# Optimization experiments

Measured on AMD Instinct MI355X. Metric: run time of the kernel, lower is better.

Reference implementation:

```python
import jax, jax.numpy as jnp
import numpy as np

B, S, D, H = 4, 2048, 1024, 16  # batch, seq, d_hidden, n_heads


def setup_inputs() -> dict:
    key = jax.random.key(0)
    ks = jax.random.split(key, 7)
    scale = 1.0 / np.sqrt(D)
    return {
        "x": jax.random.normal(ks[0], (B, S, D), dtype=jnp.float32),
        "Wq": jax.random.normal(ks[1], (D, D), dtype=jnp.float32) * scale,
        "bq": jax.random.normal(ks[2], (D,), dtype=jnp.float32) * 0.02,
        "Wk": jax.random.normal(ks[3], (D, D), dtype=jnp.float32) * scale,
        "bk": jax.random.normal(ks[4], (D,), dtype=jnp.float32) * 0.02,
        "Wv": jax.random.normal(ks[5], (D, D), dtype=jnp.float32) * scale,
        "bv": jax.random.normal(ks[6], (D,), dtype=jnp.float32) * 0.02,
    }


def reference(x, Wq, bq, Wk, bk, Wv, bv):
    n_heads = H
    head_dim = D // n_heads

    def proj(inp, W, b):
        # torch nn.Linear: y = x @ W^T + b
        y = jnp.einsum("bsd,ed->bse", inp, W) + b
        # split last dim into (H, Wd) then transpose to (B, H, S, Wd)
        return y.reshape(inp.shape[0], inp.shape[1], n_heads, head_dim).transpose(0, 2, 1, 3)

    q = proj(x, Wq, bq)
    k = proj(x, Wk, bk)
    v = proj(x, Wv, bv)

    # scores: (B, H, S, S)
    scores = jnp.einsum("bhqd,bhkd->bhqk", q, k) / jnp.sqrt(jnp.asarray(head_dim, q.dtype))
    attn = jax.nn.softmax(scores, axis=-1)
    h = jnp.einsum("bhqk,bhkd->bhqd", attn, v)  # (B, H, S, Wd)
    h = h.transpose(0, 2, 1, 3).reshape(x.shape[0], x.shape[1], D)  # merge heads
    return h
```

## Files before the change

### kernel.cpp

```cpp
#include <hip/hip_runtime.h>
#include <hip/hip_bf16.h>

#define B_ 4
#define S_ 2048
#define D_ 1024
#define H_ 16
#define HD 64

typedef __bf16 bf16;
typedef __bf16 bf16x4 __attribute__((ext_vector_type(4)));
typedef __bf16 bf16x8 __attribute__((ext_vector_type(8)));
typedef float f32x4 __attribute__((ext_vector_type(4)));
typedef float f32x16 __attribute__((ext_vector_type(16)));

#define LOG2E 1.4426950408889634f

__device__ inline void gload_lds16(const bf16* g, bf16* l) {
    __builtin_amdgcn_global_load_lds(
        (const __attribute__((address_space(1))) void*)g,
        (__attribute__((address_space(3))) void*)l, 16, 0, 0);
}

__device__ inline int swz(int row, int colb) {
    return row * 64 + ((colb ^ ((row & 7) << 4)) >> 1);
}

__device__ inline unsigned cvt_pk_bf16(float lo, float hi) {
    unsigned r;
    asm("v_cvt_pk_bf16_f32 %0, %1, %2" : "=v"(r) : "v"(lo), "v"(hi));
    return r;
}

__global__ void cast_pack_kernel(const float* __restrict__ x,
                                 const float* __restrict__ Wq,
                                 const float* __restrict__ Wk,
                                 const float* __restrict__ Wv,
                                 bf16* __restrict__ Xb, bf16* __restrict__ Wb) {
    const long XN = (long)B_ * S_ * D_;
    const long WN = (long)D_ * D_;
    long i4 = ((long)blockIdx.x * blockDim.x + threadIdx.x) * 4;
    if (i4 < XN) {
        float4 v = *(const float4*)(x + i4);
        bf16* o = Xb + i4;
        o[0] = (bf16)v.x; o[1] = (bf16)v.y; o[2] = (bf16)v.z; o[3] = (bf16)v.w;
    } else {
        long j = i4 - XN;
        if (j < 3 * WN) {
            int which = (int)(j / WN);
            long jj = j - (long)which * WN;
            const float* src = which == 0 ? Wq : which == 1 ? Wk : Wv;
            float4 v = *(const float4*)(src + jj);
            bf16* o = Wb + j;
            o[0] = (bf16)v.x; o[1] = (bf16)v.y; o[2] = (bf16)v.z; o[3] = (bf16)v.w;
        }
    }
}

#define TM 128
#define TN 256
#define TK 64

__global__ __launch_bounds__(512, 2) void gemm_qkv_kernel(
    const bf16* __restrict__ Xb, const bf16* __restrict__ Wb,
    const float* __restrict__ bq, const float* __restrict__ bk,
    const float* __restrict__ bv,
    bf16* __restrict__ Qg, bf16* __restrict__ Kg, bf16* __restrict__ Vt) {
    __shared__ bf16 SMEM[49152];
    bf16* As = SMEM;
    bf16* Bs = SMEM + 16384;
    const int tid = threadIdx.x;
    const int lane = tid & 63;
    const int wid = tid >> 6;
    const int col = lane & 15, grp = lane >> 4;
    const int wr = wid >> 2, wc = wid & 3;

    const int id = blockIdx.x;
    const int id2 = (id & 7) * 96 + (id >> 3);
    const int m0 = (id2 / 12) * TM;
    const int n0 = (id2 % 12) * TN;

    const int r8 = tid >> 3;
    const int cbs = ((tid & 7) * 16) ^ ((r8 & 7) << 4);
    const bf16* asrc = Xb + (size_t)(m0 + r8) * D_ + (cbs >> 1);
    const bf16* bsrc = Wb + (size_t)(n0 + r8) * D_ + (cbs >> 1);

#define STAGE_A(c, kt, j) \
    gload_lds16(asrc + (size_t)(j) * 64 * D_ + (kt) * TK, As + (c) * 8192 + (j) * 4096 + wid * 512)
#define STAGE_B(c, kt, j) \
    gload_lds16(bsrc + (size_t)(j) * 64 * D_ + (kt) * TK, Bs + (c) * 16384 + (j) * 4096 + wid * 512)

    const f32x4 zf = {0.f, 0.f, 0.f, 0.f};
    f32x4 acc[4][4];
#pragma unroll
    for (int m = 0; m < 4; m++)
#pragma unroll
        for (int n = 0; n < 4; n++) acc[m][n] = zf;

    STAGE_A(0, 0, 0); STAGE_A(0, 0, 1);
    STAGE_B(0, 0, 0); STAGE_B(0, 0, 1); STAGE_B(0, 0, 2); STAGE_B(0, 0, 3);
    asm volatile("s_waitcnt vmcnt(0)");
    __builtin_amdgcn_s_barrier();

    int c = 0;
#pragma unroll 1
    for (int kt = 0; kt < D_ / TK; ++kt) {
        const bf16* Ac = As + c * 8192;
        const bf16* Bc = Bs + c * 16384;
        {
            bf16x8 a[4], b[4];
#pragma unroll
            for (int m = 0; m < 4; m++)
                a[m] = *(const bf16x8*)(Ac + swz(wr * 64 + m * 16 + col, grp * 16));
#pragma unroll
            for (int n = 0; n < 4; n++)
                b[n] = *(const bf16x8*)(Bc + swz(wc * 64 + n * 16 + col, grp * 16));
            if (kt < D_ / TK - 1) {
                STAGE_A(c ^ 1, kt + 1, 0); STAGE_A(c ^ 1, kt + 1, 1);
                STAGE_B(c ^ 1, kt + 1, 0);
            }
            __builtin_amdgcn_s_barrier();
            asm volatile("s_waitcnt lgkmcnt(0)");
            __builtin_amdgcn_sched_barrier(0);
            __builtin_amdgcn_s_setprio(1);
#pragma unroll
            for (int m = 0; m < 4; m++)
#pragma unroll
                for (int n = 0; n < 4; n++)
                    acc[m][n] = __builtin_amdgcn_mfma_f32_16x16x32_bf16(a[m], b[n], acc[m][n], 0, 0, 0);
            __builtin_amdgcn_s_setprio(0);
            __builtin_amdgcn_s_barrier();
        }
        {
            bf16x8 a[4], b[4];
#pragma unroll
            for (int m = 0; m < 4; m++)
                a[m] = *(const bf16x8*)(Ac + swz(wr * 64 + m * 16 + col, 64 + grp * 16));
#pragma unroll
            for (int n = 0; n < 4; n++)
                b[n] = *(const bf16x8*)(Bc + swz(wc * 64 + n * 16 + col, 64 + grp * 16));
            if (kt < D_ / TK - 1) {
                STAGE_B(c ^ 1, kt + 1, 1); STAGE_B(c ^ 1, kt + 1, 2); STAGE_B(c ^ 1, kt + 1, 3);
            }
            __builtin_amdgcn_s_barrier();
            asm volatile("s_waitcnt lgkmcnt(0)");
            __builtin_amdgcn_sched_barrier(0);
            __builtin_amdgcn_s_setprio(1);
#pragma unroll
            for (int m = 0; m < 4; m++)
#pragma unroll
                for (int n = 0; n < 4; n++)
                    acc[m][n] = __builtin_amdgcn_mfma_f32_16x16x32_bf16(a[m], b[n], acc[m][n], 0, 0, 0);
            __builtin_amdgcn_s_setprio(0);
            asm volatile("s_waitcnt vmcnt(0)");
            __builtin_amdgcn_s_barrier();
        }
        c ^= 1;
    }
#undef STAGE_A
#undef STAGE_B

    const int which = n0 >> 10;
    if (which == 2) {
        __syncthreads();
        bf16* Vl = SMEM;
#pragma unroll
        for (int n = 0; n < 4; n++) {
            int dl = wc * 64 + n * 16 + col;
            float bias = bv[(n0 - 2048) + dl];
#pragma unroll
            for (int m = 0; m < 4; m++) {
                bf16x4 pv;
#pragma unroll
                for (int i = 0; i < 4; i++) pv[i] = (bf16)(acc[m][n][i] + bias);
                int sl = wr * 64 + m * 16 + grp * 4;
                *(bf16x4*)(&Vl[dl * 128 + (sl ^ ((dl & 7) << 3))]) = pv;
            }
        }
        __syncthreads();
#pragma unroll
        for (int c0 = 0; c0 < 8; c0++) {
            int cc = c0 * 512 + tid;
            int dl = cc >> 4, s8 = (cc & 15) * 8;
            bf16x8 val = *(const bf16x8*)(&Vl[dl * 128 + (s8 ^ ((dl & 7) << 3))]);
            int s = m0 + s8;
            int b = s >> 11, sl = s & 2047;
            int dglob = (n0 - 2048) + dl;
            int h = dglob >> 6, dd = dglob & 63;
            *(bf16x8*)(&Vt[((size_t)(b * H_ + h) * HD + dd) * S_ + sl]) = val;
        }
    } else {
        const float* bp = which == 0 ? bq : bk;
        bf16* dst = which == 0 ? Qg : Kg;
        const float qsc = which == 0 ? (0.125f * LOG2E) : 1.0f;
#pragma unroll
        for (int n = 0; n < 4; n++) {
            int e = n0 + wc * 64 + n * 16 + col;
            int ee = e & 1023;
            float bias = bp[ee];
            int h = ee >> 6, d = ee & 63;
#pragma unroll
            for (int m = 0; m < 4; m++) {
#pragma unroll
                for (int i = 0; i < 4; i++) {
                    int s = m0 + wr * 64 + m * 16 + grp * 4 + i;
                    int b = s >> 11, sl = s & 2047;
                    dst[((size_t)(b * H_ + h) * S_ + sl) * HD + d] =
                        (bf16)((acc[m][n][i] + bias) * qsc);
                }
            }
        }
    }
}

#define KB 64

__global__ __launch_bounds__(256, 4) void attn_kernel(
    const bf16* __restrict__ Qg, const bf16* __restrict__ Kg,
    const bf16* __restrict__ Vt, float* __restrict__ out) {
    __shared__ bf16 Ks[2][64 * 64];
    __shared__ bf16 Vs[2][64 * 64];
    const int tid = threadIdx.x, lane = tid & 63, wid = tid >> 6;
    const int l31 = lane & 31, hi = lane >> 5;

    const int id = blockIdx.x;
    const int swzid = (id & 7) * 128 + (id >> 3);
    const int bh = swzid >> 4;
    const int q0 = (swzid & 15) * 128 + wid * 32;

    const bf16* Kbase = Kg + (size_t)bh * S_ * HD;
    const bf16* Vbase = Vt + (size_t)bh * HD * S_;

    const int r0 = tid >> 3;
    const int cb = ((tid & 7) * 16) ^ ((r0 & 7) << 4);
    const bf16* ksrc = Kbase + (size_t)r0 * HD + (cb >> 1);
    const bf16* vsrc = Vbase + (size_t)r0 * S_ + (cb >> 1);

#define STAGE(bsel, kv0)                                                       \
    do {                                                                       \
        gload_lds16(ksrc + (size_t)(kv0)*HD,        &Ks[bsel][wid * 512]);     \
        gload_lds16(ksrc + (size_t)((kv0) + 32)*HD, &Ks[bsel][2048 + wid * 512]); \
        gload_lds16(vsrc + (kv0),                   &Vs[bsel][wid * 512]);     \
        gload_lds16(vsrc + 32 * S_ + (kv0),         &Vs[bsel][2048 + wid * 512]); \
    } while (0)

    bf16x8 qa[4];
#pragma unroll
    for (int ks = 0; ks < 4; ks++)
        qa[ks] = *(const bf16x8*)(Qg + ((size_t)bh * S_ + q0 + l31) * HD + ks * 16 + hi * 8);

    const f32x16 z16 = {0.f, 0.f, 0.f, 0.f, 0.f, 0.f, 0.f, 0.f,
                        0.f, 0.f, 0.f, 0.f, 0.f, 0.f, 0.f, 0.f};
    f32x16 o[2];
    o[0] = z16; o[1] = z16;
    f32x4 ls = {0.f, 0.f, 0.f, 0.f};

    int cur = 0;
    STAGE(0, 0);
    __syncthreads();

#pragma unroll 1
    for (int t = 0; t < S_ / KB; ++t) {
        if (t < S_ / KB - 1) STAGE(cur ^ 1, (t + 1) * KB);

        f32x16 sc[2];
        __builtin_amdgcn_s_setprio(1);
#pragma unroll
        for (int kvt = 0; kvt < 2; kvt++) {
#pragma unroll
            for (int ks = 0; ks < 4; ks++) {
                bf16x8 kb = *(const bf16x8*)(&Ks[cur][swz(kvt * 32 + l31, ks * 32 + hi * 16)]);
                if (ks == 0)
                    sc[kvt] = __builtin_amdgcn_mfma_f32_32x32x16_bf16(kb, qa[0], z16, 0, 0, 0);
                else
                    sc[kvt] = __builtin_amdgcn_mfma_f32_32x32x16_bf16(kb, qa[ks], sc[kvt], 0, 0, 0);
            }
        }
        __builtin_amdgcn_s_setprio(0);

#pragma unroll
        for (int kvt = 0; kvt < 2; kvt++) {
            float p[16];
#pragma unroll
            for (int r = 0; r < 16; r++) p[r] = __builtin_amdgcn_exp2f(sc[kvt][r]);
            f32x4 s0 = {p[0], p[1], p[2], p[3]};
            f32x4 s1 = {p[4], p[5], p[6], p[7]};
            f32x4 s2 = {p[8], p[9], p[10], p[11]};
            f32x4 s3 = {p[12], p[13], p[14], p[15]};
            ls += (s0 + s1) + (s2 + s3);
            bf16x8 pa[2];
#pragma unroll
            for (int b = 0; b < 2; b++) {
                unsigned A  = cvt_pk_bf16(p[8 * b + 0], p[8 * b + 1]);
                unsigned Bw = cvt_pk_bf16(p[8 * b + 4], p[8 * b + 5]);
                unsigned C  = cvt_pk_bf16(p[8 * b + 2], p[8 * b + 3]);
                unsigned Dw = cvt_pk_bf16(p[8 * b + 6], p[8 * b + 7]);
                asm("v_permlane32_swap_b32 %0, %1" : "+v"(A), "+v"(Bw));
                asm("v_permlane32_swap_b32 %0, %1" : "+v"(C), "+v"(Dw));
                union { unsigned u[4]; bf16x8 v; } pk;
                pk.u[0] = A; pk.u[1] = C; pk.u[2] = Bw; pk.u[3] = Dw;
                pa[b] = pk.v;
            }
            __builtin_amdgcn_s_setprio(1);
#pragma unroll
            for (int b = 0; b < 2; b++) {
                int kk = kvt * 2 + b;
                bf16x8 vb0 = *(const bf16x8*)(&Vs[cur][swz(l31,      kk * 32 + hi * 16)]);
                bf16x8 vb1 = *(const bf16x8*)(&Vs[cur][swz(32 + l31, kk * 32 + hi * 16)]);
                o[0] = __builtin_amdgcn_mfma_f32_32x32x16_bf16(vb0, pa[b], o[0], 0, 0, 0);
                o[1] = __builtin_amdgcn_mfma_f32_32x32x16_bf16(vb1, pa[b], o[1], 0, 0, 0);
            }
            __builtin_amdgcn_s_setprio(0);
        }

        __syncthreads();
        cur ^= 1;
    }

    float denom = ls[0] + ls[1] + ls[2] + ls[3];
    denom += __shfl_xor(denom, 32);
    float inv = 1.f / denom;

    int b = bh >> 4, h = bh & 15;
    int q = q0 + l31;
    float* obase = out + ((size_t)(b * S_ + q)) * D_ + h * HD;
#pragma unroll
    for (int dt = 0; dt < 2; dt++)
#pragma unroll
        for (int g = 0; g < 4; g++) {
            f32x4 r = {o[dt][4 * g + 0] * inv, o[dt][4 * g + 1] * inv,
                       o[dt][4 * g + 2] * inv, o[dt][4 * g + 3] * inv};
            *(f32x4*)(obase + dt * 32 + 8 * g + 4 * hi) = r;
        }
#undef STAGE
}

extern "C" void kernel_launch(void* const* d_in, const int* in_sizes, int n_in,
                              void* d_out, int out_size, void* d_ws, size_t ws_size,
                              hipStream_t stream) {
    const float* x  = (const float*)d_in[0];
    const float* Wq = (const float*)d_in[1];
    const float* bq = (const float*)d_in[2];
    const float* Wk = (const float*)d_in[3];
    const float* bk = (const float*)d_in[4];
    const float* Wv = (const float*)d_in[5];
    const float* bv = (const float*)d_in[6];
    float* out = (float*)d_out;

    bf16* ws = (bf16*)d_ws;
    bf16* Xb = ws;
    bf16* Wb = Xb + (size_t)B_ * S_ * D_;
    bf16* Qg = Wb + (size_t)3 * D_ * D_;
    bf16* Kg = Qg + (size_t)B_ * S_ * D_;
    bf16* Vt = Kg + (size_t)B_ * S_ * D_;

    hipLaunchKernelGGL(cast_pack_kernel,
                       dim3((B_ * S_ * D_ + 3 * D_ * D_) / (4 * 256)), dim3(256), 0, stream,
                       x, Wq, Wk, Wv, Xb, Wb);
    hipLaunchKernelGGL(gemm_qkv_kernel, dim3(64 * 12), dim3(512), 0, stream,
                       Xb, Wb, bq, bk, bv, Qg, Kg, Vt);
    hipLaunchKernelGGL(attn_kernel, dim3(1024), dim3(256), 0, stream,
                       Qg, Kg, Vt, out);
}
```

Baseline: 163.6 us.

## Triple-buffer QKV GEMM loads with two-stage prefetch and fewer barriers

Replaces the double-buffered K-loop of the QKV projection GEMM with a three-stage LDS ring that prefetches two tiles ahead. Each iteration now issues all six async global-to-LDS loads at once, waits with vmcnt(6), and uses one barrier instead of several per step. The loop is fully unrolled. This raises LDS use to about 144KB per block, which likely prevents two blocks from sharing a CU and reduces occupancy.

```diff
diff --git a/kernel.cpp b/kernel.cpp
--- a/kernel.cpp
+++ b/kernel.cpp
@@ -59,15 +59,16 @@
 #define TM 128
 #define TN 256
 #define TK 64
+#define NKT (D_ / TK)
 
 __global__ __launch_bounds__(512, 2) void gemm_qkv_kernel(
     const bf16* __restrict__ Xb, const bf16* __restrict__ Wb,
     const float* __restrict__ bq, const float* __restrict__ bk,
     const float* __restrict__ bv,
     bf16* __restrict__ Qg, bf16* __restrict__ Kg, bf16* __restrict__ Vt) {
-    __shared__ bf16 SMEM[49152];
+    __shared__ bf16 SMEM[73728];
     bf16* As = SMEM;
-    bf16* Bs = SMEM + 16384;
+    bf16* Bs = SMEM + 3 * 8192;
     const int tid = threadIdx.x;
     const int lane = tid & 63;
     const int wid = tid >> 6;
@@ -84,10 +85,15 @@
     const bf16* asrc = Xb + (size_t)(m0 + r8) * D_ + (cbs >> 1);
     const bf16* bsrc = Wb + (size_t)(n0 + r8) * D_ + (cbs >> 1);
 
-#define STAGE_A(c, kt, j) \
-    gload_lds16(asrc + (size_t)(j) * 64 * D_ + (kt) * TK, As + (c) * 8192 + (j) * 4096 + wid * 512)
-#define STAGE_B(c, kt, j) \
-    gload_lds16(bsrc + (size_t)(j) * 64 * D_ + (kt) * TK, Bs + (c) * 16384 + (j) * 4096 + wid * 512)
+#define STAGE_ALL(c, kt)                                                                    \
+    do {                                                                                    \
+        gload_lds16(asrc + (kt) * TK,                       As + (c) * 8192 + wid * 512);   \
+        gload_lds16(asrc + (size_t)64 * D_ + (kt) * TK,     As + (c) * 8192 + 4096 + wid * 512); \
+        gload_lds16(bsrc + (kt) * TK,                       Bs + (c) * 16384 + wid * 512);  \
+        gload_lds16(bsrc + (size_t)64 * D_ + (kt) * TK,     Bs + (c) * 16384 + 4096 + wid * 512); \
+        gload_lds16(bsrc + (size_t)128 * D_ + (kt) * TK,    Bs + (c) * 16384 + 8192 + wid * 512); \
+        gload_lds16(bsrc + (size_t)192 * D_ + (kt) * TK,    Bs + (c) * 16384 + 12288 + wid * 512); \
+    } while (0)
 
     const f32x4 zf = {0.f, 0.f, 0.f, 0.f};
     f32x4 acc[4][4];
@@ -96,68 +102,51 @@
 #pragma unroll
         for (int n = 0; n < 4; n++) acc[m][n] = zf;
 
-    STAGE_A(0, 0, 0); STAGE_A(0, 0, 1);
-    STAGE_B(0, 0, 0); STAGE_B(0, 0, 1); STAGE_B(0, 0, 2); STAGE_B(0, 0, 3);
-    asm volatile("s_waitcnt vmcnt(0)");
+    STAGE_ALL(0, 0);
+    STAGE_ALL(1, 1);
+    asm volatile("s_waitcnt vmcnt(6)" ::: "memory");
     __builtin_amdgcn_s_barrier();
 
-    int c = 0;
-#pragma unroll 1
-    for (int kt = 0; kt < D_ / TK; ++kt) {
+#pragma unroll
+    for (int kt = 0; kt < NKT; ++kt) {
+        const int c = kt % 3;
         const bf16* Ac = As + c * 8192;
         const bf16* Bc = Bs + c * 16384;
-        {
-            bf16x8 a[4], b[4];
-#pragma unroll
-            for (int m = 0; m < 4; m++)
-                a[m] = *(const bf16x8*)(Ac + swz(wr * 64 + m * 16 + col, grp * 16));
+
+        bf16x8 a0[4], b0[4], a1[4], b1[4];
+#pragma unroll
+        for (int m = 0; m < 4; m++) {
+            a0[m] = *(const bf16x8*)(Ac + swz(wr * 64 + m * 16 + col, grp * 16));
+            a1[m] = *(const bf16x8*)(Ac + swz(wr * 64 + m * 16 + col, 64 + grp * 16));
+        }
+#pragma unroll
+        for (int n = 0; n < 4; n++) {
+            b0[n] = *(const bf16x8*)(Bc + swz(wc * 64 + n * 16 + col, grp * 16));
+            b1[n] = *(const bf16x8*)(Bc + swz(wc * 64 + n * 16 + col, 64 + grp * 16));
+        }
+
+        if (kt < NKT - 2) STAGE_ALL((kt + 2) % 3, kt + 2);
+
+        __builtin_amdgcn_s_setprio(1);
+#pragma unroll
+        for (int m = 0; m < 4; m++)
 #pragma unroll
             for (int n = 0; n < 4; n++)
-                b[n] = *(const bf16x8*)(Bc + swz(wc * 64 + n * 16 + col, grp * 16));
-            if (kt < D_ / TK - 1) {
-                STAGE_A(c ^ 1, kt + 1, 0); STAGE_A(c ^ 1, kt + 1, 1);
-                STAGE_B(c ^ 1, kt + 1, 0);
-            }
-            __builtin_amdgcn_s_barrier();
-            asm volatile("s_waitcnt lgkmcnt(0)");
-            __builtin_amdgcn_sched_barrier(0);
-            __builtin_amdgcn_s_setprio(1);
-#pragma unroll
-            for (int m = 0; m < 4; m++)
-#pragma unroll
-                for (int n = 0; n < 4; n++)
-                    acc[m][n] = __builtin_amdgcn_mfma_f32_16x16x32_bf16(a[m], b[n], acc[m][n], 0, 0, 0);
-            __builtin_amdgcn_s_setprio(0);
-            __builtin_amdgcn_s_barrier();
-        }
-        {
-            bf16x8 a[4], b[4];
-#pragma unroll
-            for (int m = 0; m < 4; m++)
-                a[m] = *(const bf16x8*)(Ac + swz(wr * 64 + m * 16 + col, 64 + grp * 16));
+                acc[m][n] = __builtin_amdgcn_mfma_f32_16x16x32_bf16(a0[m], b0[n], acc[m][n], 0, 0, 0);
+#pragma unroll
+        for (int m = 0; m < 4; m++)
 #pragma unroll
             for (int n = 0; n < 4; n++)
-                b[n] = *(const bf16x8*)(Bc + swz(wc * 64 + n * 16 + col, 64 + grp * 16));
-            if (kt < D_ / TK - 1) {
-                STAGE_B(c ^ 1, kt + 1, 1); STAGE_B(c ^ 1, kt + 1, 2); STAGE_B(c ^ 1, kt + 1, 3);
-            }
-            __builtin_amdgcn_s_barrier();
-            asm volatile("s_waitcnt lgkmcnt(0)");
-            __builtin_amdgcn_sched_barrier(0);
-            __builtin_amdgcn_s_setprio(1);
-#pragma unroll
-            for (int m = 0; m < 4; m++)
-#pragma unroll
-                for (int n = 0; n < 4; n++)
-                    acc[m][n] = __builtin_amdgcn_mfma_f32_16x16x32_bf16(a[m], b[n], acc[m][n], 0, 0, 0);
-            __builtin_amdgcn_s_setprio(0);
-            asm volatile("s_waitcnt vmcnt(0)");
-            __builtin_amdgcn_s_barrier();
-        }
-        c ^= 1;
+                acc[m][n] = __builtin_amdgcn_mfma_f32_16x16x32_bf16(a1[m], b1[n], acc[m][n], 0, 0, 0);
+        __builtin_amdgcn_s_setprio(0);
+
+        if (kt < NKT - 2)
+            asm volatile("s_waitcnt vmcnt(6)" ::: "memory");
+        else if (kt == NKT - 2)
+            asm volatile("s_waitcnt vmcnt(0)" ::: "memory");
+        __builtin_amdgcn_s_barrier();
     }
-#undef STAGE_A
-#undef STAGE_B
+#undef STAGE_ALL
 
     const int which = n0 >> 10;
     if (which == 2) {
```

Result: faster. 160.3 us (-2.0%).
